# Performance work log

Measured on AMD Instinct MI355X. Metric: run time of the kernel, lower is better.

The kernel has to match this reference:

```python
import jax, jax.numpy as jnp
import numpy as np

N_WORDS = 8192   # total words in batch (flattened ragged loop)
CHAR_LEN = 16    # chars per word (padded/fixed instance)
WORD_VOCAB = 50000
CHAR_VOCAB = 128
WORD_DIM = 300
CHAR_DIM = 64
CHAR_HID = 128   # per-direction LSTM hidden
INPUT_DIM = 512
INFO_DIM = WORD_DIM + 2 * CHAR_HID  # 556


def setup_inputs() -> dict:
    key = jax.random.key(0)
    ks = jax.random.split(key, 16)
    s_ih = 1.0 / np.sqrt(CHAR_DIM)
    s_hh = 1.0 / np.sqrt(CHAR_HID)
    s_out = 1.0 / np.sqrt(INFO_DIM)
    return {
        "word_ids": jax.random.randint(ks[0], (N_WORDS,), 0, WORD_VOCAB),
        "char_ids": jax.random.randint(ks[1], (N_WORDS, CHAR_LEN), 0, CHAR_VOCAB),
        "word_table": jax.random.normal(ks[2], (WORD_VOCAB, WORD_DIM), jnp.float32),
        "char_table": jax.random.normal(ks[3], (CHAR_VOCAB, CHAR_DIM), jnp.float32),
        "Wih_f": jax.random.uniform(ks[4], (4 * CHAR_HID, CHAR_DIM), jnp.float32, -s_ih, s_ih),
        "Whh_f": jax.random.uniform(ks[5], (4 * CHAR_HID, CHAR_HID), jnp.float32, -s_hh, s_hh),
        "bih_f": jax.random.uniform(ks[6], (4 * CHAR_HID,), jnp.float32, -s_hh, s_hh),
        "bhh_f": jax.random.uniform(ks[7], (4 * CHAR_HID,), jnp.float32, -s_hh, s_hh),
        "Wih_b": jax.random.uniform(ks[8], (4 * CHAR_HID, CHAR_DIM), jnp.float32, -s_ih, s_ih),
        "Whh_b": jax.random.uniform(ks[9], (4 * CHAR_HID, CHAR_HID), jnp.float32, -s_hh, s_hh),
        "bih_b": jax.random.uniform(ks[10], (4 * CHAR_HID,), jnp.float32, -s_hh, s_hh),
        "bhh_b": jax.random.uniform(ks[11], (4 * CHAR_HID,), jnp.float32, -s_hh, s_hh),
        "W_out": jax.random.uniform(ks[12], (INPUT_DIM, INFO_DIM), jnp.float32, -s_out, s_out),
        "b_out": jax.random.uniform(ks[13], (INPUT_DIM,), jnp.float32, -s_out, s_out),
    }


def _lstm_dir(x, Wih, Whh, bih, bhh, reverse):
    # x: [L, N, D] -> outputs [L, N, H]; PyTorch gate order i,f,g,o; zero init state.
    L, N, _ = x.shape
    H = Whh.shape[1]
    b = bih + bhh

    def step(carry, xt):
        h, c = carry
        gates = xt @ Wih.T + h @ Whh.T + b  # [N, 4H]
        i, f, g, o = jnp.split(gates, 4, axis=-1)
        c = jax.nn.sigmoid(f) * c + jax.nn.sigmoid(i) * jnp.tanh(g)
        h = jax.nn.sigmoid(o) * jnp.tanh(c)
        return (h, c), h

    init = (jnp.zeros((N, H), x.dtype), jnp.zeros((N, H), x.dtype))
    _, hs = jax.lax.scan(step, init, x, reverse=reverse)
    return hs


def reference(word_ids, char_ids, word_table, char_table,
              Wih_f, Whh_f, bih_f, bhh_f,
              Wih_b, Whh_b, bih_b, bhh_b,
              W_out, b_out):
    w = word_table[word_ids]                     # [N, WORD_DIM]
    ce = char_table[char_ids]                    # [N, L, CHAR_DIM]
    x = jnp.transpose(ce, (1, 0, 2))             # [L, N, CHAR_DIM]
    hf = _lstm_dir(x, Wih_f, Whh_f, bih_f, bhh_f, reverse=False)  # [L, N, H]
    hb = _lstm_dir(x, Wih_b, Whh_b, bih_b, bhh_b, reverse=True)   # [L, N, H]
    # torch.sum over char positions of bidirectional outputs
    char_feat = jnp.sum(jnp.concatenate([hf, hb], axis=-1), axis=0)  # [N, 2H]
    feat = jnp.concatenate([w, char_feat], axis=-1)                  # [N, INFO_DIM]
    return jnp.tanh(feat @ W_out.T + b_out)                          # [N, INPUT_DIM]
```

## Files before the change

kernel.cpp:

```cpp
#include <hip/hip_runtime.h>
#include <hip/hip_bf16.h>

typedef __bf16 bf16x8 __attribute__((ext_vector_type(8)));
typedef float  f32x4  __attribute__((ext_vector_type(4)));

#define N_WORDS   8192
#define CHAR_LEN  16
#define WORD_DIM  300
#define CHAR_DIM  64
#define HID       128
#define G4        512
#define INFO      556
#define KPAD      576
#define OUTD      512
#define WB        16
#define L2E       1.4426950408889634f

__device__ __forceinline__ float sig_(float x) {
    return __builtin_amdgcn_rcpf(1.0f + __builtin_amdgcn_exp2f(-L2E * x));
}
__device__ __forceinline__ float tanh_(float x) {
    return 1.0f - 2.0f * __builtin_amdgcn_rcpf(1.0f + __builtin_amdgcn_exp2f((2.0f * L2E) * x));
}

__global__ void pre_kernel(const float* __restrict__ char_table,
                           const float* __restrict__ Wih_f, const float* __restrict__ bih_f,
                           const float* __restrict__ bhh_f,
                           const float* __restrict__ Wih_b, const float* __restrict__ bih_b,
                           const float* __restrict__ bhh_b,
                           float* __restrict__ preT) {
    const int dir = blockIdx.y;
    const int cid = blockIdx.x;
    const float* Wih = dir ? Wih_b : Wih_f;
    const float* b1  = dir ? bih_b : bih_f;
    const float* b2  = dir ? bhh_b : bhh_f;
    __shared__ float x[CHAR_DIM];
    if (threadIdx.x < CHAR_DIM) x[threadIdx.x] = char_table[cid * CHAR_DIM + threadIdx.x];
    __syncthreads();
    for (int g = threadIdx.x; g < G4; g += 256) {
        const f32x4* w4 = (const f32x4*)(Wih + g * CHAR_DIM);
        const f32x4* x4 = (const f32x4*)x;
        float s = b1[g] + b2[g];
        #pragma unroll
        for (int d = 0; d < CHAR_DIM / 4; ++d) {
            f32x4 wv = w4[d], xv = x4[d];
            s += wv[0]*xv[0] + wv[1]*xv[1] + wv[2]*xv[2] + wv[3]*xv[3];
        }
        int tt = g >> 7, j = g & (HID - 1);
        preT[(dir * 128 + cid) * G4 + j * 4 + tt] = s;
    }
}

__global__ void prep_kernel(const float* __restrict__ W_out,
                            const float* __restrict__ Whh_f, const float* __restrict__ Whh_b,
                            __bf16* __restrict__ Wpad, __bf16* __restrict__ WhhB) {
    int idx = blockIdx.x * 256 + threadIdx.x;
    if (idx < OUTD * KPAD) {
        int row = idx / KPAD, col = idx - row * KPAD;
        Wpad[idx] = (col < INFO) ? (__bf16)W_out[row * INFO + col] : (__bf16)0.0f;
    } else {
        int j = idx - OUTD * KPAD;
        if (j < 2 * G4 * HID) {
            const float* src = (j < G4 * HID) ? Whh_f : Whh_b;
            int k = (j < G4 * HID) ? j : j - G4 * HID;
            WhhB[j] = (__bf16)src[k];
        }
    }
}

__global__ __launch_bounds__(512, 4) void lstm_kernel(
        const int*   __restrict__ char_ids,
        const float* __restrict__ preT,
        const __bf16* __restrict__ WhhB,
        __bf16* __restrict__ char_feat) {
    const int dir = blockIdx.y;
    const int wb  = blockIdx.x * WB;
    const __bf16* Whh = WhhB + dir * G4 * HID;
    const float* preD = preT + dir * 128 * G4;

    const int tid  = threadIdx.x;
    const int wave = tid >> 6;
    const int lane = tid & 63;
    const int col  = lane & 15;
    const int quad = lane >> 4;
    const int jbase = wave * 16;

    __shared__ __bf16 h_lds[2][WB][136];
    __shared__ int    cid_lds[WB][CHAR_LEN];

    if (tid < WB * CHAR_LEN) {
        int w = tid >> 4, t = tid & 15;
        cid_lds[w][t] = char_ids[(wb + w) * CHAR_LEN + t];
    }
    for (int i = tid; i < 2 * WB * 136; i += 512) ((__bf16*)h_lds)[i] = (__bf16)0.0f;

    bf16x8 Bfrag[4][4];
    #pragma unroll
    for (int tt = 0; tt < 4; ++tt) {
        int row = tt * HID + jbase + col;
        #pragma unroll
        for (int ks = 0; ks < 4; ++ks)
            Bfrag[tt][ks] = *(const bf16x8*)(Whh + row * HID + ks * 32 + quad * 8);
    }

    float c[4] = {}, sumh[4] = {};

    __syncthreads();

    f32x4 nx[4];
    {
        const int tc0 = dir ? (CHAR_LEN - 1) : 0;
        #pragma unroll
        for (int r = 0; r < 4; ++r)
            nx[r] = *(const f32x4*)(preD + cid_lds[quad * 4 + r][tc0] * G4 + (jbase + col) * 4);
    }

    for (int t = 0; t < CHAR_LEN; ++t) {
        const __bf16 (*hc)[136] = h_lds[t & 1];
        __bf16 (*hn)[136] = h_lds[(t + 1) & 1];

        f32x4 acc[4];
        #pragma unroll
        for (int tt = 0; tt < 4; ++tt)
            acc[tt] = (f32x4){nx[0][tt], nx[1][tt], nx[2][tt], nx[3][tt]};

        bf16x8 A = *(const bf16x8*)(&hc[col][quad * 8]);
        #pragma unroll
        for (int tt = 0; tt < 4; ++tt)
            acc[tt] = __builtin_amdgcn_mfma_f32_16x16x32_bf16(A, Bfrag[tt][0], acc[tt], 0, 0, 0);

        if (t + 1 < CHAR_LEN) {
            const int tc = dir ? (CHAR_LEN - 2 - t) : (t + 1);
            #pragma unroll
            for (int r = 0; r < 4; ++r)
                nx[r] = *(const f32x4*)(preD + cid_lds[quad * 4 + r][tc] * G4 + (jbase + col) * 4);
        }

        #pragma unroll
        for (int ks = 1; ks < 4; ++ks) {
            A = *(const bf16x8*)(&hc[col][ks * 32 + quad * 8]);
            #pragma unroll
            for (int tt = 0; tt < 4; ++tt)
                acc[tt] = __builtin_amdgcn_mfma_f32_16x16x32_bf16(A, Bfrag[tt][ks], acc[tt], 0, 0, 0);
        }

        #pragma unroll
        for (int r = 0; r < 4; ++r) {
            float iv = sig_(acc[0][r]);
            float fv = sig_(acc[1][r]);
            float gv = tanh_(acc[2][r]);
            float ov = sig_(acc[3][r]);
            float cv = fv * c[r] + iv * gv;
            c[r] = cv;
            float hv = ov * tanh_(cv);
            sumh[r] += hv;
            hn[quad * 4 + r][jbase + col] = (__bf16)hv;
        }
        __syncthreads();
    }

    #pragma unroll
    for (int r = 0; r < 4; ++r)
        char_feat[(wb + quad * 4 + r) * 256 + dir * HID + jbase + col] = (__bf16)sumh[r];
}

__global__ __launch_bounds__(256, 4) void out_kernel(
        const int*   __restrict__ word_ids,
        const float* __restrict__ word_table,
        const __bf16* __restrict__ char_feat,
        const __bf16* __restrict__ Wpad,
        const float* __restrict__ b_out,
        float* __restrict__ out) {
    const int wb  = blockIdx.x * WB;
    const int tid = threadIdx.x;
    const int wave = tid >> 6, lane = tid & 63, col = lane & 15, quad = lane >> 4;

    __shared__ __bf16 feat[WB][584];
    __shared__ int wid[WB];
    if (tid < WB) wid[tid] = word_ids[wb + tid];
    __syncthreads();
    for (int idx = tid; idx < WB * 75; idx += 256) {
        int row = idx / 75, ch = idx - row * 75;
        f32x4 v = *(const f32x4*)(word_table + wid[row] * WORD_DIM + ch * 4);
        __bf16* d = &feat[row][ch * 4];
        d[0] = (__bf16)v[0]; d[1] = (__bf16)v[1]; d[2] = (__bf16)v[2]; d[3] = (__bf16)v[3];
    }
    for (int idx = tid; idx < WB * 32; idx += 256) {
        int row = idx / 32, ch = idx - row * 32;
        bf16x8 v = *(const bf16x8*)(char_feat + (wb + row) * 256 + ch * 8);
        __bf16* d = &feat[row][WORD_DIM + ch * 8];
        #pragma unroll
        for (int e = 0; e < 8; ++e) d[e] = v[e];
    }
    for (int idx = tid; idx < WB * 28; idx += 256) {
        int row = idx / 28, cc = idx - row * 28;
        feat[row][INFO + cc] = (__bf16)0.0f;
    }
    __syncthreads();

    f32x4 acc[8];
    #pragma unroll
    for (int nt = 0; nt < 8; ++nt) acc[nt] = (f32x4){0.f, 0.f, 0.f, 0.f};

    for (int kb = 0; kb < KPAD / 32; ++kb) {
        bf16x8 A = *(const bf16x8*)(&feat[col][kb * 32 + quad * 8]);
        #pragma unroll
        for (int nt = 0; nt < 8; ++nt) {
            int n = wave * 128 + nt * 16 + col;
            bf16x8 B = *(const bf16x8*)(Wpad + n * KPAD + kb * 32 + quad * 8);
            acc[nt] = __builtin_amdgcn_mfma_f32_16x16x32_bf16(A, B, acc[nt], 0, 0, 0);
        }
    }

    #pragma unroll
    for (int nt = 0; nt < 8; ++nt) {
        int n = wave * 128 + nt * 16 + col;
        float bo = b_out[n];
        #pragma unroll
        for (int r = 0; r < 4; ++r) {
            int word = wb + quad * 4 + r;
            out[word * OUTD + n] = tanh_(acc[nt][r] + bo);
        }
    }
}

extern "C" void kernel_launch(void* const* d_in, const int* in_sizes, int n_in,
                              void* d_out, int out_size, void* d_ws, size_t ws_size,
                              hipStream_t stream) {
    const int*   word_ids   = (const int*)d_in[0];
    const int*   char_ids   = (const int*)d_in[1];
    const float* word_table = (const float*)d_in[2];
    const float* char_table = (const float*)d_in[3];
    const float* Wih_f = (const float*)d_in[4];
    const float* Whh_f = (const float*)d_in[5];
    const float* bih_f = (const float*)d_in[6];
    const float* bhh_f = (const float*)d_in[7];
    const float* Wih_b = (const float*)d_in[8];
    const float* Whh_b = (const float*)d_in[9];
    const float* bih_b = (const float*)d_in[10];
    const float* bhh_b = (const float*)d_in[11];
    const float* W_out = (const float*)d_in[12];
    const float* b_out = (const float*)d_in[13];

    char* ws = (char*)d_ws;
    float*  preT      = (float*)ws;
    __bf16* WhhB      = (__bf16*)(ws + 524288);
    __bf16* Wpad      = (__bf16*)(ws + 524288 + 262144);
    __bf16* char_feat = (__bf16*)(ws + 524288 + 262144 + 589824);

    prep_kernel<<<(OUTD * KPAD + 2 * G4 * HID + 255) / 256, 256, 0, stream>>>(
        W_out, Whh_f, Whh_b, Wpad, WhhB);
    pre_kernel<<<dim3(128, 2), 256, 0, stream>>>(char_table, Wih_f, bih_f, bhh_f,
                                                 Wih_b, bih_b, bhh_b, preT);
    lstm_kernel<<<dim3(N_WORDS / WB, 2), 512, 0, stream>>>(char_ids, preT, WhhB, char_feat);
    out_kernel<<<N_WORDS / WB, 256, 0, stream>>>(word_ids, word_table, char_feat, Wpad, b_out,
                                                 (float*)d_out);
}
```

Baseline: 221.6 us.

## Process 32 words per LSTM block and merge the prep kernels into one launch

The LSTM kernel now handles 32 words per block as two 16-row M tiles. Each wave reuses its register-resident Whh fragments across twice as many MFMAs per step, and the number of per-step barriers per word is halved. Char ids are stored transposed and pre-scaled to byte offsets, so the preT gather needs one vector LDS read per four rows. The two setup kernels are merged into a single launch, and the out_kernel K loop is unrolled by 2. The cost is more registers (launch bounds drop to 2 blocks per CU) and half as many LSTM blocks, which may reduce latency hiding on the serial recurrence.

```diff
diff --git a/kernel.cpp b/kernel.cpp
--- a/kernel.cpp
+++ b/kernel.cpp
@@ -3,6 +3,7 @@
 
 typedef __bf16 bf16x8 __attribute__((ext_vector_type(8)));
 typedef float  f32x4  __attribute__((ext_vector_type(4)));
+typedef int    i32x4  __attribute__((ext_vector_type(4)));
 
 #define N_WORDS   8192
 #define CHAR_LEN  16
@@ -13,6 +14,7 @@
 #define INFO      556
 #define KPAD      576
 #define OUTD      512
+#define WBL       32
 #define WB        16
 #define L2E       1.4426950408889634f
 
@@ -23,58 +25,59 @@
     return 1.0f - 2.0f * __builtin_amdgcn_rcpf(1.0f + __builtin_amdgcn_exp2f((2.0f * L2E) * x));
 }
 
-__global__ void pre_kernel(const float* __restrict__ char_table,
-                           const float* __restrict__ Wih_f, const float* __restrict__ bih_f,
-                           const float* __restrict__ bhh_f,
-                           const float* __restrict__ Wih_b, const float* __restrict__ bih_b,
-                           const float* __restrict__ bhh_b,
-                           float* __restrict__ preT) {
-    const int dir = blockIdx.y;
-    const int cid = blockIdx.x;
-    const float* Wih = dir ? Wih_b : Wih_f;
-    const float* b1  = dir ? bih_b : bih_f;
-    const float* b2  = dir ? bhh_b : bhh_f;
+__global__ void prep_kernel(const float* __restrict__ char_table,
+                            const float* __restrict__ Wih_f, const float* __restrict__ bih_f,
+                            const float* __restrict__ bhh_f,
+                            const float* __restrict__ Wih_b, const float* __restrict__ bih_b,
+                            const float* __restrict__ bhh_b,
+                            const float* __restrict__ W_out,
+                            const float* __restrict__ Whh_f, const float* __restrict__ Whh_b,
+                            float* __restrict__ preT,
+                            __bf16* __restrict__ Wpad, __bf16* __restrict__ WhhB) {
     __shared__ float x[CHAR_DIM];
-    if (threadIdx.x < CHAR_DIM) x[threadIdx.x] = char_table[cid * CHAR_DIM + threadIdx.x];
-    __syncthreads();
-    for (int g = threadIdx.x; g < G4; g += 256) {
-        const f32x4* w4 = (const f32x4*)(Wih + g * CHAR_DIM);
-        const f32x4* x4 = (const f32x4*)x;
-        float s = b1[g] + b2[g];
-        #pragma unroll
-        for (int d = 0; d < CHAR_DIM / 4; ++d) {
-            f32x4 wv = w4[d], xv = x4[d];
-            s += wv[0]*xv[0] + wv[1]*xv[1] + wv[2]*xv[2] + wv[3]*xv[3];
-        }
-        int tt = g >> 7, j = g & (HID - 1);
-        preT[(dir * 128 + cid) * G4 + j * 4 + tt] = s;
-    }
-}
-
-__global__ void prep_kernel(const float* __restrict__ W_out,
-                            const float* __restrict__ Whh_f, const float* __restrict__ Whh_b,
-                            __bf16* __restrict__ Wpad, __bf16* __restrict__ WhhB) {
-    int idx = blockIdx.x * 256 + threadIdx.x;
-    if (idx < OUTD * KPAD) {
-        int row = idx / KPAD, col = idx - row * KPAD;
-        Wpad[idx] = (col < INFO) ? (__bf16)W_out[row * INFO + col] : (__bf16)0.0f;
+    if (blockIdx.x < 256) {
+        const int dir = blockIdx.x & 1;
+        const int cid = blockIdx.x >> 1;
+        const float* Wih = dir ? Wih_b : Wih_f;
+        const float* b1  = dir ? bih_b : bih_f;
+        const float* b2  = dir ? bhh_b : bhh_f;
+        if (threadIdx.x < CHAR_DIM) x[threadIdx.x] = char_table[cid * CHAR_DIM + threadIdx.x];
+        __syncthreads();
+        for (int g = threadIdx.x; g < G4; g += 256) {
+            const f32x4* w4 = (const f32x4*)(Wih + g * CHAR_DIM);
+            const f32x4* x4 = (const f32x4*)x;
+            float s = b1[g] + b2[g];
+            #pragma unroll
+            for (int d = 0; d < CHAR_DIM / 4; ++d) {
+                f32x4 wv = w4[d], xv = x4[d];
+                s += wv[0]*xv[0] + wv[1]*xv[1] + wv[2]*xv[2] + wv[3]*xv[3];
+            }
+            int tt = g >> 7, j = g & (HID - 1);
+            preT[(dir * 128 + cid) * G4 + j * 4 + tt] = s;
+        }
     } else {
-        int j = idx - OUTD * KPAD;
-        if (j < 2 * G4 * HID) {
-            const float* src = (j < G4 * HID) ? Whh_f : Whh_b;
-            int k = (j < G4 * HID) ? j : j - G4 * HID;
-            WhhB[j] = (__bf16)src[k];
-        }
-    }
-}
-
-__global__ __launch_bounds__(512, 4) void lstm_kernel(
+        int idx = (blockIdx.x - 256) * 256 + threadIdx.x;
+        if (idx < OUTD * KPAD) {
+            int row = idx / KPAD, col = idx - row * KPAD;
+            Wpad[idx] = (col < INFO) ? (__bf16)W_out[row * INFO + col] : (__bf16)0.0f;
+        } else {
+            int j = idx - OUTD * KPAD;
+            if (j < 2 * G4 * HID) {
+                const float* src = (j < G4 * HID) ? Whh_f : Whh_b;
+                int k = (j < G4 * HID) ? j : j - G4 * HID;
+                WhhB[j] = (__bf16)src[k];
+            }
+        }
+    }
+}
+
+__global__ __launch_bounds__(512, 2) void lstm_kernel(
         const int*   __restrict__ char_ids,
         const float* __restrict__ preT,
         const __bf16* __restrict__ WhhB,
         __bf16* __restrict__ char_feat) {
     const int dir = blockIdx.y;
-    const int wb  = blockIdx.x * WB;
+    const int wb  = blockIdx.x * WBL;
     const __bf16* Whh = WhhB + dir * G4 * HID;
     const float* preD = preT + dir * 128 * G4;
 
@@ -85,14 +88,14 @@
     const int quad = lane >> 4;
     const int jbase = wave * 16;
 
-    __shared__ __bf16 h_lds[2][WB][136];
-    __shared__ int    cid_lds[WB][CHAR_LEN];
-
-    if (tid < WB * CHAR_LEN) {
+    __shared__ __bf16 h_lds[2][WBL][136];
+    __shared__ int    cidT[CHAR_LEN][WBL];
+
+    {
         int w = tid >> 4, t = tid & 15;
-        cid_lds[w][t] = char_ids[(wb + w) * CHAR_LEN + t];
-    }
-    for (int i = tid; i < 2 * WB * 136; i += 512) ((__bf16*)h_lds)[i] = (__bf16)0.0f;
+        cidT[t][w] = char_ids[(wb + w) * CHAR_LEN + t] * (G4 * 4);
+    }
+    for (int i = tid; i < 2 * WBL * 136; i += 512) ((__bf16*)h_lds)[i] = (__bf16)0.0f;
 
     bf16x8 Bfrag[4][4];
     #pragma unroll
@@ -103,65 +106,90 @@
             Bfrag[tt][ks] = *(const bf16x8*)(Whh + row * HID + ks * 32 + quad * 8);
     }
 
-    float c[4] = {}, sumh[4] = {};
+    const char* base_lane = (const char*)(preD + (jbase + col) * 4);
+
+    float c[2][4] = {}, sumh[2][4] = {};
 
     __syncthreads();
 
-    f32x4 nx[4];
+    f32x4 nx[2][4];
     {
         const int tc0 = dir ? (CHAR_LEN - 1) : 0;
         #pragma unroll
-        for (int r = 0; r < 4; ++r)
-            nx[r] = *(const f32x4*)(preD + cid_lds[quad * 4 + r][tc0] * G4 + (jbase + col) * 4);
+        for (int mt = 0; mt < 2; ++mt) {
+            i32x4 off = *(const i32x4*)(&cidT[tc0][mt * 16 + quad * 4]);
+            #pragma unroll
+            for (int r = 0; r < 4; ++r)
+                nx[mt][r] = *(const f32x4*)(base_lane + off[r]);
+        }
     }
 
     for (int t = 0; t < CHAR_LEN; ++t) {
         const __bf16 (*hc)[136] = h_lds[t & 1];
         __bf16 (*hn)[136] = h_lds[(t + 1) & 1];
 
-        f32x4 acc[4];
-        #pragma unroll
-        for (int tt = 0; tt < 4; ++tt)
-            acc[tt] = (f32x4){nx[0][tt], nx[1][tt], nx[2][tt], nx[3][tt]};
-
-        bf16x8 A = *(const bf16x8*)(&hc[col][quad * 8]);
-        #pragma unroll
-        for (int tt = 0; tt < 4; ++tt)
-            acc[tt] = __builtin_amdgcn_mfma_f32_16x16x32_bf16(A, Bfrag[tt][0], acc[tt], 0, 0, 0);
+        f32x4 acc[2][4];
+        #pragma unroll
+        for (int mt = 0; mt < 2; ++mt)
+            #pragma unroll
+            for (int tt = 0; tt < 4; ++tt)
+                acc[mt][tt] = (f32x4){nx[mt][0][tt], nx[mt][1][tt], nx[mt][2][tt], nx[mt][3][tt]};
+
+        {
+            bf16x8 A0 = *(const bf16x8*)(&hc[col][quad * 8]);
+            bf16x8 A1 = *(const bf16x8*)(&hc[16 + col][quad * 8]);
+            #pragma unroll
+            for (int tt = 0; tt < 4; ++tt) {
+                acc[0][tt] = __builtin_amdgcn_mfma_f32_16x16x32_bf16(A0, Bfrag[tt][0], acc[0][tt], 0, 0, 0);
+                acc[1][tt] = __builtin_amdgcn_mfma_f32_16x16x32_bf16(A1, Bfrag[tt][0], acc[1][tt], 0, 0, 0);
+            }
+        }
 
         if (t + 1 < CHAR_LEN) {
             const int tc = dir ? (CHAR_LEN - 2 - t) : (t + 1);
             #pragma unroll
-            for (int r = 0; r < 4; ++r)
-                nx[r] = *(const f32x4*)(preD + cid_lds[quad * 4 + r][tc] * G4 + (jbase + col) * 4);
+            for (int mt = 0; mt < 2; ++mt) {
+                i32x4 off = *(const i32x4*)(&cidT[tc][mt * 16 + quad * 4]);
+                #pragma unroll
+                for (int r = 0; r < 4; ++r)
+                    nx[mt][r] = *(const f32x4*)(base_lane + off[r]);
+            }
         }
 
         #pragma unroll
         for (int ks = 1; ks < 4; ++ks) {
-            A = *(const bf16x8*)(&hc[col][ks * 32 + quad * 8]);
-            #pragma unroll
-            for (int tt = 0; tt < 4; ++tt)
-                acc[tt] = __builtin_amdgcn_mfma_f32_16x16x32_bf16(A, Bfrag[tt][ks], acc[tt], 0, 0, 0);
-        }
-
-        #pragma unroll
-        for (int r = 0; r < 4; ++r) {
-            float iv = sig_(acc[0][r]);
-            float fv = sig_(acc[1][r]);
-            float gv = tanh_(acc[2][r]);
-            float ov = sig_(acc[3][r]);
-            float cv = fv * c[r] + iv * gv;
-            c[r] = cv;
-            float hv = ov * tanh_(cv);
-            sumh[r] += hv;
-            hn[quad * 4 + r][jbase + col] = (__bf16)hv;
-        }
+            bf16x8 A0 = *(const bf16x8*)(&hc[col][ks * 32 + quad * 8]);
+            bf16x8 A1 = *(const bf16x8*)(&hc[16 + col][ks * 32 + quad * 8]);
+            #pragma unroll
+            for (int tt = 0; tt < 4; ++tt) {
+                acc[0][tt] = __builtin_amdgcn_mfma_f32_16x16x32_bf16(A0, Bfrag[tt][ks], acc[0][tt], 0, 0, 0);
+                acc[1][tt] = __builtin_amdgcn_mfma_f32_16x16x32_bf16(A1, Bfrag[tt][ks], acc[1][tt], 0, 0, 0);
+            }
+        }
+
+        #pragma unroll
+        for (int mt = 0; mt < 2; ++mt)
+            #pragma unroll
+            for (int r = 0; r < 4; ++r) {
+                float iv = sig_(acc[mt][0][r]);
+                float fv = sig_(acc[mt][1][r]);
+                float gv = tanh_(acc[mt][2][r]);
+                float ov = sig_(acc[mt][3][r]);
+                float cv = fv * c[mt][r] + iv * gv;
+                c[mt][r] = cv;
+                float hv = ov * tanh_(cv);
+                sumh[mt][r] += hv;
+                hn[mt * 16 + quad * 4 + r][jbase + col] = (__bf16)hv;
+            }
         __syncthreads();
     }
 
     #pragma unroll
-    for (int r = 0; r < 4; ++r)
-        char_feat[(wb + quad * 4 + r) * 256 + dir * HID + jbase + col] = (__bf16)sumh[r];
+    for (int mt = 0; mt < 2; ++mt)
+        #pragma unroll
+        for (int r = 0; r < 4; ++r)
+            char_feat[(wb + mt * 16 + quad * 4 + r) * 256 + dir * HID + jbase + col]
+                = (__bf16)sumh[mt][r];
 }
 
 __global__ __launch_bounds__(256, 4) void out_kernel(
@@ -202,6 +230,7 @@
     #pragma unroll
     for (int nt = 0; nt < 8; ++nt) acc[nt] = (f32x4){0.f, 0.f, 0.f, 0.f};
 
+    #pragma unroll 2
     for (int kb = 0; kb < KPAD / 32; ++kb) {
         bf16x8 A = *(const bf16x8*)(&feat[col][kb * 32 + quad * 8]);
         #pragma unroll
@@ -248,11 +277,10 @@
     __bf16* Wpad      = (__bf16*)(ws + 524288 + 262144);
     __bf16* char_feat = (__bf16*)(ws + 524288 + 262144 + 589824);
 
-    prep_kernel<<<(OUTD * KPAD + 2 * G4 * HID + 255) / 256, 256, 0, stream>>>(
-        W_out, Whh_f, Whh_b, Wpad, WhhB);
-    pre_kernel<<<dim3(128, 2), 256, 0, stream>>>(char_table, Wih_f, bih_f, bhh_f,
-                                                 Wih_b, bih_b, bhh_b, preT);
-    lstm_kernel<<<dim3(N_WORDS / WB, 2), 512, 0, stream>>>(char_ids, preT, WhhB, char_feat);
+    prep_kernel<<<256 + (OUTD * KPAD + 2 * G4 * HID + 255) / 256, 256, 0, stream>>>(
+        char_table, Wih_f, bih_f, bhh_f, Wih_b, bih_b, bhh_b,
+        W_out, Whh_f, Whh_b, preT, Wpad, WhhB);
+    lstm_kernel<<<dim3(N_WORDS / WBL, 2), 512, 0, stream>>>(char_ids, preT, WhhB, char_feat);
     out_kernel<<<N_WORDS / WB, 256, 0, stream>>>(word_ids, word_table, char_feat, Wpad, b_out,
                                                  (float*)d_out);
 }
```

Result: no change. 222.2 us (+0.3%).
